# Optimization experiments

Measured on AMD Instinct MI355X. Metric: run time of the kernel, lower is better.

## Reference

```python
import jax, jax.numpy as jnp
import numpy as np

B, D, H = 32768, 512, 512


def setup_inputs() -> dict:
    key = jax.random.key(0)
    ks = jax.random.split(key, 20)
    stdv = 1.0 / np.sqrt(H)

    def u(k, shape):
        return jax.random.uniform(k, shape, jnp.float32, -stdv, stdv)

    inp = {
        "input": jax.random.normal(ks[0], (B, D), jnp.float32),
        "h": jax.random.normal(ks[1], (B, H), jnp.float32),
        "c": jax.random.normal(ks[2], (B, H), jnp.float32),
    }
    names = ["w_ii", "w_hi", "b_ii", "b_hi", "w_if", "w_hf", "b_if", "b_hf",
             "w_ig", "w_hg", "b_ig", "b_hg", "w_io", "w_ho", "b_io", "b_ho"]
    shapes = {"w_i": (D, H), "w_h": (H, H), "b_": (H,)}
    for i, n in enumerate(names):
        shp = (D, H) if n.startswith("w_i") else ((H, H) if n.startswith("w_h") else (H,))
        inp[n] = u(ks[3 + i], shp)
    return inp


def lstm_cell(input, h, c,
              w_ii, w_hi, b_ii, b_hi, w_if, w_hf, b_if, b_hf,
              w_ig, w_hg, b_ig, b_hg, w_io, w_ho, b_io, b_ho):
    # Fuse the 8 small GEMMs into 2 concatenated GEMMs: [B,D]@[D,4H], [B,H]@[H,4H].
    w_x = jnp.concatenate([w_ii, w_if, w_ig, w_io], axis=1)   # [D, 4H]
    w_h = jnp.concatenate([w_hi, w_hf, w_hg, w_ho], axis=1)   # [H, 4H]
    b = jnp.concatenate([b_ii + b_hi, b_if + b_hf, b_ig + b_hg, b_io + b_ho])  # [4H]
    pre = input @ w_x + h @ w_h + b                            # [B, 4H]
    i, f, g, o = jnp.split(pre, 4, axis=1)
    i = jax.nn.sigmoid(i)
    f = jax.nn.sigmoid(f)
    g = jax.nn.sigmoid(g)  # NOTE: source code uses sigmoid here (docstring says tanh)
    o = jax.nn.sigmoid(o)
    c_prime = f * c + i * g
    h_prime = o * jnp.tanh(c_prime)
    return h_prime, c_prime


def reference(input, h, c,
              w_ii, w_hi, b_ii, b_hi, w_if, w_hf, b_if, b_hf,
              w_ig, w_hg, b_ig, b_hg, w_io, w_ho, b_io, b_ho):
    return lstm_cell(input, h, c,
                     w_ii, w_hi, b_ii, b_hi, w_if, w_hf, b_if, b_hf,
                     w_ig, w_hg, b_ig, b_hg, w_io, w_ho, b_io, b_ho)
```

## Files before the change

### kernel.cpp

```cpp
#include <hip/hip_runtime.h>
#include <hip/hip_bf16.h>

typedef __attribute__((ext_vector_type(8))) __bf16 bf16x8;
typedef __attribute__((ext_vector_type(4))) float f32x4;

#define NB 32768
#define HDIM 512
#define KDIM 1024

struct WPtrs { const float* wi[4]; const float* wh[4]; };
struct BPtrs { const float* bi[4]; const float* bh[4]; };

__device__ __forceinline__ float fsigmoid(float x) {
  return 1.0f / (1.0f + __expf(-x));
}
__device__ __forceinline__ float ftanh(float x) {
  return 2.0f / (1.0f + __expf(-2.0f * x)) - 1.0f;
}
__device__ __forceinline__ bf16x8 pack8(float4 a, float4 b) {
  bf16x8 r;
  r[0] = (__bf16)a.x; r[1] = (__bf16)a.y; r[2] = (__bf16)a.z; r[3] = (__bf16)a.w;
  r[4] = (__bf16)b.x; r[5] = (__bf16)b.y; r[6] = (__bf16)b.z; r[7] = (__bf16)b.w;
  return r;
}
__device__ __forceinline__ void gll16(const void* g, void* l) {
  __builtin_amdgcn_global_load_lds(
      (const __attribute__((address_space(1))) void*)g,
      (__attribute__((address_space(3))) void*)l, 16, 0, 0);
}
#define MFMA16(A, B, C) \
  C = __builtin_amdgcn_mfma_f32_16x16x32_bf16(A, B, C, 0, 0, 0)

__global__ void pack_bias_kernel(BPtrs p, float* __restrict__ bias) {
  int idx = blockIdx.x * 256 + threadIdx.x;
  int g = idx >> 9, np = idx & 511;
  bias[idx] = p.bi[g][np] + p.bh[g][np];
}

__global__ void conv_a_kernel(const float* __restrict__ x,
                              const float* __restrict__ h,
                              __bf16* __restrict__ Abf) {
  const size_t N8 = (size_t)NB * KDIM / 8;
  for (size_t i = (size_t)blockIdx.x * blockDim.x + threadIdx.x; i < N8;
       i += (size_t)gridDim.x * blockDim.x) {
    size_t e = i * 8;
    int k = (int)(e & (KDIM - 1));
    size_t r = e >> 10;
    const float* s = (k < 512) ? (x + r * 512 + k) : (h + r * 512 + (k - 512));
    float4 v0 = *(const float4*)s;
    float4 v1 = *(const float4*)(s + 4);
    *(bf16x8*)(Abf + e) = pack8(v0, v1);
  }
}

__global__ void pack_w2_kernel(WPtrs p, __bf16* __restrict__ Wt) {
  __shared__ float tile[64][65];
  const int kt = blockIdx.x;
  const int nt = blockIdx.y;
  const int g = blockIdx.z;
  const int k0 = kt * 64, n0 = nt * 64;
  const float* src = (k0 < 512) ? p.wi[g] : p.wh[g];
  const int k0l = (k0 < 512) ? k0 : (k0 - 512);
  const int rr = threadIdx.x >> 6;
  const int cc = threadIdx.x & 63;
#pragma unroll
  for (int pp = 0; pp < 16; ++pp) {
    int kk = pp * 4 + rr;
    tile[kk][cc] = src[(size_t)(k0l + kk) * 512 + (n0 + cc)];
  }
  __syncthreads();
#pragma unroll
  for (int pp = 0; pp < 16; ++pp) {
    int nn = pp * 4 + rr;
    int np = n0 + nn;
    int prow = (np >> 6) * 256 + ((g >> 1) << 7) + (((np >> 4) & 3) << 5) +
               ((g & 1) << 4) + (np & 15);
    Wt[(size_t)prow * KDIM + (k0 + cc)] = (__bf16)tile[cc][nn];
  }
}

__global__ __launch_bounds__(512, 1) void lstm_gemm3(
    const __bf16* __restrict__ Abf, const __bf16* __restrict__ Wt,
    const float* __restrict__ cin, const float* __restrict__ bias,
    float* __restrict__ out) {
  __shared__ alignas(16) char lds[131072];
  const int tid = threadIdx.x;
  const int wid = tid >> 6;
  const int wm = wid >> 2, wn = wid & 3;
  const int lane = tid & 63;
  const int fc = lane & 15, fg = lane >> 4;

  const int bn = blockIdx.x & 7;
  const int bmg = blockIdx.x >> 3;

  const __bf16* Bsrc = Wt + (size_t)bn * 256 * KDIM;

  const int r0 = tid >> 3;
  const int ssl = ((tid & 7) ^ (r0 & 7)) * 8;
  const uint32_t ldst0 = (uint32_t)(tid >> 6) * 1024;

  f32x4 acc[8][4];
#pragma unroll
  for (int m = 0; m < 8; ++m)
#pragma unroll
    for (int n = 0; n < 4; ++n) acc[m][n] = (f32x4){0.f, 0.f, 0.f, 0.f};

  bf16x8 a[4][2], b0[2][2], b1[2][2];

  auto stA = [&](int t, int h) {
    if (t < 64) {
      const __bf16* g = Abf +
                        ((size_t)((bmg << 2) + (t >> 4)) * 256 + h * 128 + r0) *
                            KDIM +
                        (t & 15) * 64 + ssl;
      uint32_t lb = (uint32_t)(t & 1) * 65536 + (uint32_t)h * 16384 + ldst0;
      gll16(g, (void*)&lds[lb]);
      gll16(g + (size_t)64 * KDIM, (void*)&lds[lb + 8192]);
    }
  };
  auto stB = [&](int t, int h) {
    if (t < 64) {
      const __bf16* g =
          Bsrc + ((size_t)h * 128 + r0) * KDIM + (t & 15) * 64 + ssl;
      uint32_t lb =
          (uint32_t)(t & 1) * 65536 + 32768 + (uint32_t)h * 16384 + ldst0;
      gll16(g, (void*)&lds[lb]);
      gll16(g + (size_t)64 * KDIM, (void*)&lds[lb + 8192]);
    }
  };
  auto ldA = [&](int cb, int h, int mq, int ks) -> bf16x8 {
    int row = wm * 64 + mq * 16 + fc;
    uint32_t off = (uint32_t)cb * 65536 + (uint32_t)h * 16384 +
                   (uint32_t)row * 128 +
                   (uint32_t)(((ks * 4 + fg) ^ (row & 7)) << 4);
    return *(const bf16x8*)&lds[off];
  };
  auto ldB = [&](int cb, int h, int nq, int ks) -> bf16x8 {
    int row = wn * 32 + nq * 16 + fc;
    uint32_t off = (uint32_t)cb * 65536 + 32768 + (uint32_t)h * 16384 +
                   (uint32_t)row * 128 +
                   (uint32_t)(((ks * 4 + fg) ^ (row & 7)) << 4);
    return *(const bf16x8*)&lds[off];
  };

  const int np = bn * 64 + wn * 16 + fc;
  const float bi = bias[np];
  const float bf_ = bias[512 + np];
  const float bg = bias[1024 + np];
  const float bo = bias[1536 + np];
  const size_t couts = (size_t)NB * HDIM;

  stA(0, 0); stB(0, 0); stB(0, 1); stA(0, 1);
  stA(1, 0); stB(1, 0); stB(1, 1);
  asm volatile("s_waitcnt vmcnt(6)" ::: "memory");
  __builtin_amdgcn_s_barrier();

#pragma unroll 2
  for (int t = 0; t < 64; ++t) {
    const int cb = t & 1;
#pragma unroll
    for (int mq = 0; mq < 4; ++mq)
#pragma unroll
      for (int ks = 0; ks < 2; ++ks) a[mq][ks] = ldA(cb, 0, mq, ks);
#pragma unroll
    for (int nq = 0; nq < 2; ++nq)
#pragma unroll
      for (int ks = 0; ks < 2; ++ks) b0[nq][ks] = ldB(cb, 0, nq, ks);
    stA(t + 1, 1);
    __builtin_amdgcn_s_barrier();
    asm volatile("s_waitcnt lgkmcnt(0)" ::: "memory");
    __builtin_amdgcn_s_setprio(1);
#pragma unroll
    for (int mq = 0; mq < 4; ++mq)
#pragma unroll
      for (int nq = 0; nq < 2; ++nq)
#pragma unroll
        for (int ks = 0; ks < 2; ++ks)
          MFMA16(a[mq][ks], b0[nq][ks], acc[mq][nq]);
    __builtin_amdgcn_s_setprio(0);
    __builtin_amdgcn_s_barrier();
#pragma unroll
    for (int nq = 0; nq < 2; ++nq)
#pragma unroll
      for (int ks = 0; ks < 2; ++ks) b1[nq][ks] = ldB(cb, 1, nq, ks);
    stA(t + 2, 0);
    __builtin_amdgcn_s_barrier();
    asm volatile("s_waitcnt lgkmcnt(0)" ::: "memory");
    __builtin_amdgcn_s_setprio(1);
#pragma unroll
    for (int mq = 0; mq < 4; ++mq)
#pragma unroll
      for (int nq = 0; nq < 2; ++nq)
#pragma unroll
        for (int ks = 0; ks < 2; ++ks)
          MFMA16(a[mq][ks], b1[nq][ks], acc[mq][2 + nq]);
    __builtin_amdgcn_s_setprio(0);
    __builtin_amdgcn_s_barrier();
#pragma unroll
    for (int mq = 0; mq < 4; ++mq)
#pragma unroll
      for (int ks = 0; ks < 2; ++ks) a[mq][ks] = ldA(cb, 1, mq, ks);
    stB(t + 2, 0);
    __builtin_amdgcn_s_barrier();
    asm volatile("s_waitcnt lgkmcnt(0)" ::: "memory");
    __builtin_amdgcn_s_setprio(1);
#pragma unroll
    for (int mq = 0; mq < 4; ++mq)
#pragma unroll
      for (int nq = 0; nq < 2; ++nq)
#pragma unroll
        for (int ks = 0; ks < 2; ++ks)
          MFMA16(a[mq][ks], b1[nq][ks], acc[4 + mq][2 + nq]);
    __builtin_amdgcn_s_setprio(0);
    __builtin_amdgcn_s_barrier();
    stB(t + 2, 1);
    if (t < 62) {
      asm volatile("s_waitcnt vmcnt(6)" ::: "memory");
    } else if (t == 62) {
      asm volatile("s_waitcnt vmcnt(0)" ::: "memory");
    }
    __builtin_amdgcn_s_barrier();
    __builtin_amdgcn_s_setprio(1);
#pragma unroll
    for (int mq = 0; mq < 4; ++mq)
#pragma unroll
      for (int nq = 0; nq < 2; ++nq)
#pragma unroll
        for (int ks = 0; ks < 2; ++ks)
          MFMA16(a[mq][ks], b0[nq][ks], acc[4 + mq][nq]);
    __builtin_amdgcn_s_setprio(0);
    __builtin_amdgcn_s_barrier();

    if ((t & 15) == 15) {
      const int g = t >> 4;
#pragma unroll
      for (int mf = 0; mf < 8; ++mf) {
        const int grow0 = ((bmg << 2) + g) * 256 + (mf >> 2) * 128 + wm * 64 +
                          (mf & 3) * 16 + fg * 4;
#pragma unroll
        for (int j = 0; j < 4; ++j) {
          const size_t off = (size_t)(grow0 + j) * HDIM + np;
          float i_ = fsigmoid(acc[mf][0][j] + bi);
          float f_ = fsigmoid(acc[mf][1][j] + bf_);
          float g_ = fsigmoid(acc[mf][2][j] + bg);
          float o_ = fsigmoid(acc[mf][3][j] + bo);
          float cp = f_ * cin[off] + i_ * g_;
          out[off] = o_ * ftanh(cp);
          out[couts + off] = cp;
        }
#pragma unroll
        for (int n = 0; n < 4; ++n) acc[mf][n] = (f32x4){0.f, 0.f, 0.f, 0.f};
      }
    }
  }
}

extern "C" void kernel_launch(void* const* d_in, const int* in_sizes, int n_in,
                              void* d_out, int out_size, void* d_ws,
                              size_t ws_size, hipStream_t stream) {
  const float* xin = (const float*)d_in[0];
  const float* hin = (const float*)d_in[1];
  const float* cin = (const float*)d_in[2];
  WPtrs wp;
  wp.wi[0] = (const float*)d_in[3];
  wp.wi[1] = (const float*)d_in[7];
  wp.wi[2] = (const float*)d_in[11];
  wp.wi[3] = (const float*)d_in[15];
  wp.wh[0] = (const float*)d_in[4];
  wp.wh[1] = (const float*)d_in[8];
  wp.wh[2] = (const float*)d_in[12];
  wp.wh[3] = (const float*)d_in[16];
  BPtrs bp;
  bp.bi[0] = (const float*)d_in[5];
  bp.bi[1] = (const float*)d_in[9];
  bp.bi[2] = (const float*)d_in[13];
  bp.bi[3] = (const float*)d_in[17];
  bp.bh[0] = (const float*)d_in[6];
  bp.bh[1] = (const float*)d_in[10];
  bp.bh[2] = (const float*)d_in[14];
  bp.bh[3] = (const float*)d_in[18];

  const size_t needA = (size_t)NB * KDIM * 2;
  const size_t needW = (size_t)2048 * KDIM * 2;

  __bf16* Abf = (__bf16*)d_ws;
  __bf16* Wt = (__bf16*)((char*)d_ws + needA);
  float* bias = (float*)((char*)d_ws + needA + needW);

  conv_a_kernel<<<2048, 256, 0, stream>>>(xin, hin, Abf);
  pack_w2_kernel<<<dim3(16, 8, 4), 256, 0, stream>>>(wp, Wt);
  pack_bias_kernel<<<8, 256, 0, stream>>>(bp, bias);
  lstm_gemm3<<<256, 512, 0, stream>>>(Abf, Wt, cin, bias, (float*)d_out);
}
```

Baseline: 213.8 us.

## Restructure GEMM main loop with partial lgkmcnt waits and fewer barriers

Reorders the LDS fragment loads in the main GEMM loop so both B halves are loaded up front, then splits each MFMA phase into halves gated by partial lgkmcnt waits so compute starts before all LDS reads land. Several workgroup barriers are removed or replaced with scheduler barriers to cut synchronisation stalls per iteration. This raises register pressure (b0 and b1 live together) and relies on correct hazard ordering between LDS writes from global_load_lds and reads, which could risk races if a barrier was load-bearing.

```diff
diff --git a/kernel.cpp b/kernel.cpp
--- a/kernel.cpp
+++ b/kernel.cpp
@@ -30,6 +30,8 @@
 }
 #define MFMA16(A, B, C) \
   C = __builtin_amdgcn_mfma_f32_16x16x32_bf16(A, B, C, 0, 0, 0)
+#define SBAR() __builtin_amdgcn_s_barrier()
+#define SCHED0() __builtin_amdgcn_sched_barrier(0)
 
 __global__ void pack_bias_kernel(BPtrs p, float* __restrict__ bias) {
   int idx = blockIdx.x * 256 + threadIdx.x;
@@ -79,7 +81,7 @@
   }
 }
 
-__global__ __launch_bounds__(512, 1) void lstm_gemm3(
+__global__ __launch_bounds__(512, 1) void lstm_gemm4(
     const __bf16* __restrict__ Abf, const __bf16* __restrict__ Wt,
     const float* __restrict__ cin, const float* __restrict__ bias,
     float* __restrict__ out) {
@@ -153,22 +155,50 @@
   stA(0, 0); stB(0, 0); stB(0, 1); stA(0, 1);
   stA(1, 0); stB(1, 0); stB(1, 1);
   asm volatile("s_waitcnt vmcnt(6)" ::: "memory");
-  __builtin_amdgcn_s_barrier();
+  SBAR();
 
 #pragma unroll 2
   for (int t = 0; t < 64; ++t) {
     const int cb = t & 1;
 #pragma unroll
+    for (int nq = 0; nq < 2; ++nq)
+#pragma unroll
+      for (int ks = 0; ks < 2; ++ks) b0[nq][ks] = ldB(cb, 0, nq, ks);
+#pragma unroll
     for (int mq = 0; mq < 4; ++mq)
 #pragma unroll
       for (int ks = 0; ks < 2; ++ks) a[mq][ks] = ldA(cb, 0, mq, ks);
 #pragma unroll
     for (int nq = 0; nq < 2; ++nq)
 #pragma unroll
-      for (int ks = 0; ks < 2; ++ks) b0[nq][ks] = ldB(cb, 0, nq, ks);
+      for (int ks = 0; ks < 2; ++ks) b1[nq][ks] = ldB(cb, 1, nq, ks);
     stA(t + 1, 1);
-    __builtin_amdgcn_s_barrier();
+    asm volatile("s_waitcnt lgkmcnt(8)" ::: "memory");
+    SCHED0();
+    __builtin_amdgcn_s_setprio(1);
+#pragma unroll
+    for (int mq = 0; mq < 2; ++mq)
+#pragma unroll
+      for (int nq = 0; nq < 2; ++nq)
+#pragma unroll
+        for (int ks = 0; ks < 2; ++ks)
+          MFMA16(a[mq][ks], b0[nq][ks], acc[mq][nq]);
+    __builtin_amdgcn_s_setprio(0);
+    asm volatile("s_waitcnt lgkmcnt(4)" ::: "memory");
+    SCHED0();
+    __builtin_amdgcn_s_setprio(1);
+#pragma unroll
+    for (int mq = 2; mq < 4; ++mq)
+#pragma unroll
+      for (int nq = 0; nq < 2; ++nq)
+#pragma unroll
+        for (int ks = 0; ks < 2; ++ks)
+          MFMA16(a[mq][ks], b0[nq][ks], acc[mq][nq]);
+    __builtin_amdgcn_s_setprio(0);
+    SBAR();
+    stA(t + 2, 0);
     asm volatile("s_waitcnt lgkmcnt(0)" ::: "memory");
+    SCHED0();
     __builtin_amdgcn_s_setprio(1);
 #pragma unroll
     for (int mq = 0; mq < 4; ++mq)
@@ -176,50 +206,45 @@
       for (int nq = 0; nq < 2; ++nq)
 #pragma unroll
         for (int ks = 0; ks < 2; ++ks)
-          MFMA16(a[mq][ks], b0[nq][ks], acc[mq][nq]);
-    __builtin_amdgcn_s_setprio(0);
-    __builtin_amdgcn_s_barrier();
-#pragma unroll
-    for (int nq = 0; nq < 2; ++nq)
-#pragma unroll
-      for (int ks = 0; ks < 2; ++ks) b1[nq][ks] = ldB(cb, 1, nq, ks);
-    stA(t + 2, 0);
-    __builtin_amdgcn_s_barrier();
+          MFMA16(a[mq][ks], b1[nq][ks], acc[mq][2 + nq]);
+    __builtin_amdgcn_s_setprio(0);
+#pragma unroll
+    for (int mq = 0; mq < 4; ++mq)
+#pragma unroll
+      for (int ks = 0; ks < 2; ++ks) a[mq][ks] = ldA(cb, 1, mq, ks);
+    SCHED0();
+    SBAR();
+    stB(t + 2, 0);
+    asm volatile("s_waitcnt lgkmcnt(4)" ::: "memory");
+    SCHED0();
+    __builtin_amdgcn_s_setprio(1);
+#pragma unroll
+    for (int mq = 0; mq < 2; ++mq)
+#pragma unroll
+      for (int nq = 0; nq < 2; ++nq)
+#pragma unroll
+        for (int ks = 0; ks < 2; ++ks)
+          MFMA16(a[mq][ks], b1[nq][ks], acc[4 + mq][2 + nq]);
+    __builtin_amdgcn_s_setprio(0);
     asm volatile("s_waitcnt lgkmcnt(0)" ::: "memory");
-    __builtin_amdgcn_s_setprio(1);
-#pragma unroll
-    for (int mq = 0; mq < 4; ++mq)
-#pragma unroll
-      for (int nq = 0; nq < 2; ++nq)
-#pragma unroll
-        for (int ks = 0; ks < 2; ++ks)
-          MFMA16(a[mq][ks], b1[nq][ks], acc[mq][2 + nq]);
-    __builtin_amdgcn_s_setprio(0);
-    __builtin_amdgcn_s_barrier();
-#pragma unroll
-    for (int mq = 0; mq < 4; ++mq)
-#pragma unroll
-      for (int ks = 0; ks < 2; ++ks) a[mq][ks] = ldA(cb, 1, mq, ks);
-    stB(t + 2, 0);
-    __builtin_amdgcn_s_barrier();
-    asm volatile("s_waitcnt lgkmcnt(0)" ::: "memory");
-    __builtin_amdgcn_s_setprio(1);
-#pragma unroll
-    for (int mq = 0; mq < 4; ++mq)
+    SCHED0();
+    __builtin_amdgcn_s_setprio(1);
+#pragma unroll
+    for (int mq = 2; mq < 4; ++mq)
 #pragma unroll
       for (int nq = 0; nq < 2; ++nq)
 #pragma unroll
         for (int ks = 0; ks < 2; ++ks)
           MFMA16(a[mq][ks], b1[nq][ks], acc[4 + mq][2 + nq]);
     __builtin_amdgcn_s_setprio(0);
-    __builtin_amdgcn_s_barrier();
+    SBAR();
     stB(t + 2, 1);
     if (t < 62) {
       asm volatile("s_waitcnt vmcnt(6)" ::: "memory");
     } else if (t == 62) {
       asm volatile("s_waitcnt vmcnt(0)" ::: "memory");
     }
-    __builtin_amdgcn_s_barrier();
+    SCHED0();
     __builtin_amdgcn_s_setprio(1);
 #pragma unroll
     for (int mq = 0; mq < 4; ++mq)
@@ -229,7 +254,7 @@
         for (int ks = 0; ks < 2; ++ks)
           MFMA16(a[mq][ks], b0[nq][ks], acc[4 + mq][nq]);
     __builtin_amdgcn_s_setprio(0);
-    __builtin_amdgcn_s_barrier();
+    SBAR();
 
     if ((t & 15) == 15) {
       const int g = t >> 4;
@@ -290,5 +315,5 @@
   conv_a_kernel<<<2048, 256, 0, stream>>>(xin, hin, Abf);
   pack_w2_kernel<<<dim3(16, 8, 4), 256, 0, stream>>>(wp, Wt);
   pack_bias_kernel<<<8, 256, 0, stream>>>(bp, bias);
-  lstm_gemm3<<<256, 512, 0, stream>>>(Abf, Wt, cin, bias, (float*)d_out);
-}
+  lstm_gemm4<<<256, 512, 0, stream>>>(Abf, Wt, cin, bias, (float*)d_out);
+}
```

After: 210.7 us. About the same (-1.5%).

## Restructure GEMM main loop to 4-stage K=32 pipeline with interleaved LDS reads

Applied to the files above, without the earlier changes.

Replaces the two-buffer K=64 pipeline, which had four barrier-separated MFMA phases per step, with a four-buffer ring of K=32 tiles. Each step has a single barrier, and A-fragment LDS reads are interleaved with MFMA groups using fine-grained lgkmcnt waits and sched_barrier. The aim is to cut barrier count and let LDS latency hide behind MFMAs, with global prefetches issued mid-loop two stages ahead. The LDS layout drops the XOR swizzle for a plain 64-byte row stride, which may bring bank conflicts.

```diff
diff --git a/kernel.cpp b/kernel.cpp
--- a/kernel.cpp
+++ b/kernel.cpp
@@ -30,6 +30,8 @@
 }
 #define MFMA16(A, B, C) \
   C = __builtin_amdgcn_mfma_f32_16x16x32_bf16(A, B, C, 0, 0, 0)
+#define SBAR() __builtin_amdgcn_s_barrier()
+#define SCHED0() __builtin_amdgcn_sched_barrier(0)
 
 __global__ void pack_bias_kernel(BPtrs p, float* __restrict__ bias) {
   int idx = blockIdx.x * 256 + threadIdx.x;
@@ -79,7 +81,7 @@
   }
 }
 
-__global__ __launch_bounds__(512, 1) void lstm_gemm3(
+__global__ __launch_bounds__(512, 1) void lstm_gemm6(
     const __bf16* __restrict__ Abf, const __bf16* __restrict__ Wt,
     const float* __restrict__ cin, const float* __restrict__ bias,
     float* __restrict__ out) {
@@ -93,11 +95,10 @@
   const int bn = blockIdx.x & 7;
   const int bmg = blockIdx.x >> 3;
 
-  const __bf16* Bsrc = Wt + (size_t)bn * 256 * KDIM;
-
-  const int r0 = tid >> 3;
-  const int ssl = ((tid & 7) ^ (r0 & 7)) * 8;
-  const uint32_t ldst0 = (uint32_t)(tid >> 6) * 1024;
+  const __bf16* Bsrc = Wt + (size_t)(bn * 256) * KDIM;
+
+  const int srow = (wid << 4) + (lane >> 2);
+  const int skoff = (lane & 3) * 8;
 
   f32x4 acc[8][4];
 #pragma unroll
@@ -105,42 +106,36 @@
 #pragma unroll
     for (int n = 0; n < 4; ++n) acc[m][n] = (f32x4){0.f, 0.f, 0.f, 0.f};
 
-  bf16x8 a[4][2], b0[2][2], b1[2][2];
-
-  auto stA = [&](int t, int h) {
-    if (t < 64) {
-      const __bf16* g = Abf +
-                        ((size_t)((bmg << 2) + (t >> 4)) * 256 + h * 128 + r0) *
-                            KDIM +
-                        (t & 15) * 64 + ssl;
-      uint32_t lb = (uint32_t)(t & 1) * 65536 + (uint32_t)h * 16384 + ldst0;
-      gll16(g, (void*)&lds[lb]);
-      gll16(g + (size_t)64 * KDIM, (void*)&lds[lb + 8192]);
-    }
-  };
-  auto stB = [&](int t, int h) {
-    if (t < 64) {
-      const __bf16* g =
-          Bsrc + ((size_t)h * 128 + r0) * KDIM + (t & 15) * 64 + ssl;
-      uint32_t lb =
-          (uint32_t)(t & 1) * 65536 + 32768 + (uint32_t)h * 16384 + ldst0;
-      gll16(g, (void*)&lds[lb]);
-      gll16(g + (size_t)64 * KDIM, (void*)&lds[lb + 8192]);
-    }
-  };
-  auto ldA = [&](int cb, int h, int mq, int ks) -> bf16x8 {
-    int row = wm * 64 + mq * 16 + fc;
-    uint32_t off = (uint32_t)cb * 65536 + (uint32_t)h * 16384 +
-                   (uint32_t)row * 128 +
-                   (uint32_t)(((ks * 4 + fg) ^ (row & 7)) << 4);
-    return *(const bf16x8*)&lds[off];
-  };
-  auto ldB = [&](int cb, int h, int nq, int ks) -> bf16x8 {
-    int row = wn * 32 + nq * 16 + fc;
-    uint32_t off = (uint32_t)cb * 65536 + 32768 + (uint32_t)h * 16384 +
-                   (uint32_t)row * 128 +
-                   (uint32_t)(((ks * 4 + fg) ^ (row & 7)) << 4);
-    return *(const bf16x8*)&lds[off];
+  bf16x8 a[2], b[4];
+
+  auto stA = [&](int t) {
+    if (t < 128) {
+      const __bf16* s = Abf +
+                        ((size_t)((bmg << 2) + (t >> 5)) * 256 + srow) * KDIM +
+                        (t & 31) * 32 + skoff;
+      uint32_t lb = (uint32_t)(t & 3) * 32768 + (uint32_t)wid * 1024;
+      gll16(s, (void*)&lds[lb]);
+      gll16(s + (size_t)128 * KDIM, (void*)&lds[lb + 8192]);
+    }
+  };
+  auto stB = [&](int t) {
+    if (t < 128) {
+      const __bf16* s = Bsrc + (size_t)srow * KDIM + (t & 31) * 32 + skoff;
+      uint32_t lb = (uint32_t)(t & 3) * 32768 + 16384 + (uint32_t)wid * 1024;
+      gll16(s, (void*)&lds[lb]);
+      gll16(s + (size_t)128 * KDIM, (void*)&lds[lb + 8192]);
+    }
+  };
+  auto ldA = [&](uint32_t t3, int mq) -> bf16x8 {
+    return *(const bf16x8*)&lds[t3 +
+                                (uint32_t)(wm * 128 + mq * 16 + fc) * 64 +
+                                (uint32_t)fg * 16];
+  };
+  auto ldB = [&](uint32_t t3, int nq) -> bf16x8 {
+    return *(const bf16x8*)&lds[t3 + 16384 +
+                                (uint32_t)((nq >> 1) * 128 + wn * 32 +
+                                           (nq & 1) * 16 + fc) * 64 +
+                                (uint32_t)fg * 16];
   };
 
   const int np = bn * 64 + wn * 16 + fc;
@@ -150,93 +145,49 @@
   const float bo = bias[1536 + np];
   const size_t couts = (size_t)NB * HDIM;
 
-  stA(0, 0); stB(0, 0); stB(0, 1); stA(0, 1);
-  stA(1, 0); stB(1, 0); stB(1, 1);
-  asm volatile("s_waitcnt vmcnt(6)" ::: "memory");
-  __builtin_amdgcn_s_barrier();
-
-#pragma unroll 2
-  for (int t = 0; t < 64; ++t) {
-    const int cb = t & 1;
-#pragma unroll
-    for (int mq = 0; mq < 4; ++mq)
-#pragma unroll
-      for (int ks = 0; ks < 2; ++ks) a[mq][ks] = ldA(cb, 0, mq, ks);
-#pragma unroll
-    for (int nq = 0; nq < 2; ++nq)
-#pragma unroll
-      for (int ks = 0; ks < 2; ++ks) b0[nq][ks] = ldB(cb, 0, nq, ks);
-    stA(t + 1, 1);
-    __builtin_amdgcn_s_barrier();
-    asm volatile("s_waitcnt lgkmcnt(0)" ::: "memory");
-    __builtin_amdgcn_s_setprio(1);
-#pragma unroll
-    for (int mq = 0; mq < 4; ++mq)
-#pragma unroll
-      for (int nq = 0; nq < 2; ++nq)
-#pragma unroll
-        for (int ks = 0; ks < 2; ++ks)
-          MFMA16(a[mq][ks], b0[nq][ks], acc[mq][nq]);
-    __builtin_amdgcn_s_setprio(0);
-    __builtin_amdgcn_s_barrier();
-#pragma unroll
-    for (int nq = 0; nq < 2; ++nq)
-#pragma unroll
-      for (int ks = 0; ks < 2; ++ks) b1[nq][ks] = ldB(cb, 1, nq, ks);
-    stA(t + 2, 0);
-    __builtin_amdgcn_s_barrier();
-    asm volatile("s_waitcnt lgkmcnt(0)" ::: "memory");
-    __builtin_amdgcn_s_setprio(1);
-#pragma unroll
-    for (int mq = 0; mq < 4; ++mq)
-#pragma unroll
-      for (int nq = 0; nq < 2; ++nq)
-#pragma unroll
-        for (int ks = 0; ks < 2; ++ks)
-          MFMA16(a[mq][ks], b1[nq][ks], acc[mq][2 + nq]);
-    __builtin_amdgcn_s_setprio(0);
-    __builtin_amdgcn_s_barrier();
-#pragma unroll
-    for (int mq = 0; mq < 4; ++mq)
-#pragma unroll
-      for (int ks = 0; ks < 2; ++ks) a[mq][ks] = ldA(cb, 1, mq, ks);
-    stB(t + 2, 0);
-    __builtin_amdgcn_s_barrier();
-    asm volatile("s_waitcnt lgkmcnt(0)" ::: "memory");
-    __builtin_amdgcn_s_setprio(1);
-#pragma unroll
-    for (int mq = 0; mq < 4; ++mq)
-#pragma unroll
-      for (int nq = 0; nq < 2; ++nq)
-#pragma unroll
-        for (int ks = 0; ks < 2; ++ks)
-          MFMA16(a[mq][ks], b1[nq][ks], acc[4 + mq][2 + nq]);
-    __builtin_amdgcn_s_setprio(0);
-    __builtin_amdgcn_s_barrier();
-    stB(t + 2, 1);
-    if (t < 62) {
-      asm volatile("s_waitcnt vmcnt(6)" ::: "memory");
-    } else if (t == 62) {
+  stA(0); stB(0); stA(1); stB(1);
+  asm volatile("s_waitcnt vmcnt(4)" ::: "memory");
+  SBAR();
+
+#pragma unroll 4
+  for (int t = 0; t < 128; ++t) {
+    const uint32_t t3 = (uint32_t)(t & 3) * 32768;
+    a[0] = ldA(t3, 0);
+    b[0] = ldB(t3, 0);
+    b[1] = ldB(t3, 1);
+    b[2] = ldB(t3, 2);
+    b[3] = ldB(t3, 3);
+    a[1] = ldA(t3, 1);
+#pragma unroll
+    for (int mq = 0; mq < 8; ++mq) {
+      if (mq < 7) {
+        asm volatile("s_waitcnt lgkmcnt(1)" ::: "memory");
+      } else {
+        asm volatile("s_waitcnt lgkmcnt(0)" ::: "memory");
+      }
+      SCHED0();
+      __builtin_amdgcn_s_setprio(1);
+      MFMA16(a[mq & 1], b[0], acc[mq][0]);
+      MFMA16(a[mq & 1], b[1], acc[mq][1]);
+      MFMA16(a[mq & 1], b[2], acc[mq][2]);
+      MFMA16(a[mq & 1], b[3], acc[mq][3]);
+      __builtin_amdgcn_s_setprio(0);
+      if (mq < 6) a[mq & 1] = ldA(t3, mq + 2);
+      if (mq == 2) stA(t + 2);
+      if (mq == 4) stB(t + 2);
+    }
+    if (t < 126) {
+      asm volatile("s_waitcnt vmcnt(4)" ::: "memory");
+    } else if (t == 126) {
       asm volatile("s_waitcnt vmcnt(0)" ::: "memory");
     }
-    __builtin_amdgcn_s_barrier();
-    __builtin_amdgcn_s_setprio(1);
-#pragma unroll
-    for (int mq = 0; mq < 4; ++mq)
-#pragma unroll
-      for (int nq = 0; nq < 2; ++nq)
-#pragma unroll
-        for (int ks = 0; ks < 2; ++ks)
-          MFMA16(a[mq][ks], b0[nq][ks], acc[4 + mq][nq]);
-    __builtin_amdgcn_s_setprio(0);
-    __builtin_amdgcn_s_barrier();
-
-    if ((t & 15) == 15) {
-      const int g = t >> 4;
+    SBAR();
+
+    if ((t & 31) == 31) {
+      const int grp = t >> 5;
 #pragma unroll
       for (int mf = 0; mf < 8; ++mf) {
-        const int grow0 = ((bmg << 2) + g) * 256 + (mf >> 2) * 128 + wm * 64 +
-                          (mf & 3) * 16 + fg * 4;
+        const int grow0 = ((bmg << 2) + grp) * 256 + wm * 128 + mf * 16 + fg * 4;
 #pragma unroll
         for (int j = 0; j < 4; ++j) {
           const size_t off = (size_t)(grow0 + j) * HDIM + np;
@@ -290,5 +241,5 @@
   conv_a_kernel<<<2048, 256, 0, stream>>>(xin, hin, Abf);
   pack_w2_kernel<<<dim3(16, 8, 4), 256, 0, stream>>>(wp, Wt);
   pack_bias_kernel<<<8, 256, 0, stream>>>(bp, bias);
-  lstm_gemm3<<<256, 512, 0, stream>>>(Abf, Wt, cin, bias, (float*)d_out);
-}
+  lstm_gemm6<<<256, 512, 0, stream>>>(Abf, Wt, cin, bias, (float*)d_out);
+}
```

Measured after the change: 213.8 us. Within noise of the previous version (+0.0%).

## Switch GEMM to 32x32x16 MFMA with 4x2 wave tiling and simpler pipeline

Applied to the files above, without the earlier changes.

Replaces the 16x16x32 bf16 MFMA tiles with 32x32x16 MFMAs and changes the wave layout from 2x4 to 4x2. Each wave now covers 64 rows and 32 columns across all four gates. The weight packing permutation is adjusted so each 32-column group holds all four gates contiguously. The main loop is restructured to issue global-to-LDS loads for the next tile in one stage, interleave LDS reads with MFMAs using lgkmcnt waits, and use a single barrier per iteration instead of many. The aim is fewer LDS reads per FLOP and less barrier overhead. The cost is reduced prefetch depth (one tile ahead, with a full vmcnt(0) wait every iteration) and a different epilogue row mapping.

```diff
diff --git a/kernel.cpp b/kernel.cpp
--- a/kernel.cpp
+++ b/kernel.cpp
@@ -3,6 +3,7 @@
 
 typedef __attribute__((ext_vector_type(8))) __bf16 bf16x8;
 typedef __attribute__((ext_vector_type(4))) float f32x4;
+typedef __attribute__((ext_vector_type(16))) float f32x16;
 
 #define NB 32768
 #define HDIM 512
@@ -28,8 +29,12 @@
       (const __attribute__((address_space(1))) void*)g,
       (__attribute__((address_space(3))) void*)l, 16, 0, 0);
 }
-#define MFMA16(A, B, C) \
-  C = __builtin_amdgcn_mfma_f32_16x16x32_bf16(A, B, C, 0, 0, 0)
+#define MFMA32(A, B, C) \
+  C = __builtin_amdgcn_mfma_f32_32x32x16_bf16(A, B, C, 0, 0, 0)
+#define SBAR() __builtin_amdgcn_s_barrier()
+#define SCHED0() __builtin_amdgcn_sched_barrier(0)
+#define LGKM(n) asm volatile("s_waitcnt lgkmcnt(" #n ")" ::: "memory")
+#define VMCNT0() asm volatile("s_waitcnt vmcnt(0)" ::: "memory")
 
 __global__ void pack_bias_kernel(BPtrs p, float* __restrict__ bias) {
   int idx = blockIdx.x * 256 + threadIdx.x;
@@ -53,7 +58,7 @@
   }
 }
 
-__global__ void pack_w2_kernel(WPtrs p, __bf16* __restrict__ Wt) {
+__global__ void pack_w1_kernel(WPtrs p, __bf16* __restrict__ Wt) {
   __shared__ float tile[64][65];
   const int kt = blockIdx.x;
   const int nt = blockIdx.y;
@@ -73,39 +78,40 @@
   for (int pp = 0; pp < 16; ++pp) {
     int nn = pp * 4 + rr;
     int np = n0 + nn;
-    int prow = (np >> 6) * 256 + ((g >> 1) << 7) + (((np >> 4) & 3) << 5) +
-               ((g & 1) << 4) + (np & 15);
+    int prow = ((np >> 5) << 7) + g * 32 + (np & 31);
     Wt[(size_t)prow * KDIM + (k0 + cc)] = (__bf16)tile[cc][nn];
   }
 }
 
-__global__ __launch_bounds__(512, 1) void lstm_gemm3(
+__global__ __launch_bounds__(512, 1) void lstm_gemm9(
     const __bf16* __restrict__ Abf, const __bf16* __restrict__ Wt,
     const float* __restrict__ cin, const float* __restrict__ bias,
     float* __restrict__ out) {
   __shared__ alignas(16) char lds[131072];
   const int tid = threadIdx.x;
   const int wid = tid >> 6;
-  const int wm = wid >> 2, wn = wid & 3;
+  const int wm = wid >> 1, wn = wid & 1;
   const int lane = tid & 63;
-  const int fc = lane & 15, fg = lane >> 4;
+  const int l31 = lane & 31, kg = lane >> 5;
 
   const int bn = blockIdx.x & 7;
   const int bmg = blockIdx.x >> 3;
 
-  const __bf16* Bsrc = Wt + (size_t)bn * 256 * KDIM;
+  const __bf16* Bsrc = Wt + (size_t)(bn * 256) * KDIM;
 
   const int r0 = tid >> 3;
   const int ssl = ((tid & 7) ^ (r0 & 7)) * 8;
-  const uint32_t ldst0 = (uint32_t)(tid >> 6) * 1024;
-
-  f32x4 acc[8][4];
-#pragma unroll
-  for (int m = 0; m < 8; ++m)
-#pragma unroll
-    for (int n = 0; n < 4; ++n) acc[m][n] = (f32x4){0.f, 0.f, 0.f, 0.f};
-
-  bf16x8 a[4][2], b0[2][2], b1[2][2];
+  const uint32_t ldst0 = (uint32_t)wid * 1024;
+
+  f32x16 acc[2][4];
+#pragma unroll
+  for (int m = 0; m < 2; ++m)
+#pragma unroll
+    for (int g = 0; g < 4; ++g)
+#pragma unroll
+      for (int r = 0; r < 16; ++r) acc[m][g][r] = 0.f;
+
+  bf16x8 aa[2][2], bb[2][4];
 
   auto stA = [&](int t, int h) {
     if (t < 64) {
@@ -128,128 +134,103 @@
       gll16(g + (size_t)64 * KDIM, (void*)&lds[lb + 8192]);
     }
   };
-  auto ldA = [&](int cb, int h, int mq, int ks) -> bf16x8 {
-    int row = wm * 64 + mq * 16 + fc;
+  auto ldA = [&](int cb, int m, int ks) -> bf16x8 {
+    int row = wm * 64 + m * 32 + l31;
+    int h = row >> 7, lr = row & 127;
     uint32_t off = (uint32_t)cb * 65536 + (uint32_t)h * 16384 +
-                   (uint32_t)row * 128 +
-                   (uint32_t)(((ks * 4 + fg) ^ (row & 7)) << 4);
+                   (uint32_t)lr * 128 +
+                   (uint32_t)(((ks * 2 + kg) ^ (lr & 7)) << 4);
     return *(const bf16x8*)&lds[off];
   };
-  auto ldB = [&](int cb, int h, int nq, int ks) -> bf16x8 {
-    int row = wn * 32 + nq * 16 + fc;
-    uint32_t off = (uint32_t)cb * 65536 + 32768 + (uint32_t)h * 16384 +
-                   (uint32_t)row * 128 +
-                   (uint32_t)(((ks * 4 + fg) ^ (row & 7)) << 4);
+  auto ldB = [&](int cb, int g, int ks) -> bf16x8 {
+    int lr = g * 32 + l31;
+    uint32_t off = (uint32_t)cb * 65536 + 32768 + (uint32_t)wn * 16384 +
+                   (uint32_t)lr * 128 +
+                   (uint32_t)(((ks * 2 + kg) ^ (lr & 7)) << 4);
     return *(const bf16x8*)&lds[off];
   };
 
-  const int np = bn * 64 + wn * 16 + fc;
+  const int np = bn * 64 + wn * 32 + l31;
   const float bi = bias[np];
   const float bf_ = bias[512 + np];
   const float bg = bias[1024 + np];
   const float bo = bias[1536 + np];
   const size_t couts = (size_t)NB * HDIM;
 
-  stA(0, 0); stB(0, 0); stB(0, 1); stA(0, 1);
-  stA(1, 0); stB(1, 0); stB(1, 1);
-  asm volatile("s_waitcnt vmcnt(6)" ::: "memory");
-  __builtin_amdgcn_s_barrier();
+  stA(0, 0); stA(0, 1); stB(0, 0); stB(0, 1);
+  VMCNT0();
+  SBAR();
 
 #pragma unroll 2
   for (int t = 0; t < 64; ++t) {
     const int cb = t & 1;
-#pragma unroll
-    for (int mq = 0; mq < 4; ++mq)
-#pragma unroll
-      for (int ks = 0; ks < 2; ++ks) a[mq][ks] = ldA(cb, 0, mq, ks);
-#pragma unroll
-    for (int nq = 0; nq < 2; ++nq)
-#pragma unroll
-      for (int ks = 0; ks < 2; ++ks) b0[nq][ks] = ldB(cb, 0, nq, ks);
-    stA(t + 1, 1);
-    __builtin_amdgcn_s_barrier();
-    asm volatile("s_waitcnt lgkmcnt(0)" ::: "memory");
-    __builtin_amdgcn_s_setprio(1);
-#pragma unroll
-    for (int mq = 0; mq < 4; ++mq)
-#pragma unroll
-      for (int nq = 0; nq < 2; ++nq)
-#pragma unroll
-        for (int ks = 0; ks < 2; ++ks)
-          MFMA16(a[mq][ks], b0[nq][ks], acc[mq][nq]);
-    __builtin_amdgcn_s_setprio(0);
-    __builtin_amdgcn_s_barrier();
-#pragma unroll
-    for (int nq = 0; nq < 2; ++nq)
-#pragma unroll
-      for (int ks = 0; ks < 2; ++ks) b1[nq][ks] = ldB(cb, 1, nq, ks);
-    stA(t + 2, 0);
-    __builtin_amdgcn_s_barrier();
-    asm volatile("s_waitcnt lgkmcnt(0)" ::: "memory");
-    __builtin_amdgcn_s_setprio(1);
-#pragma unroll
-    for (int mq = 0; mq < 4; ++mq)
-#pragma unroll
-      for (int nq = 0; nq < 2; ++nq)
-#pragma unroll
-        for (int ks = 0; ks < 2; ++ks)
-          MFMA16(a[mq][ks], b1[nq][ks], acc[mq][2 + nq]);
-    __builtin_amdgcn_s_setprio(0);
-    __builtin_amdgcn_s_barrier();
-#pragma unroll
-    for (int mq = 0; mq < 4; ++mq)
-#pragma unroll
-      for (int ks = 0; ks < 2; ++ks) a[mq][ks] = ldA(cb, 1, mq, ks);
-    stB(t + 2, 0);
-    __builtin_amdgcn_s_barrier();
-    asm volatile("s_waitcnt lgkmcnt(0)" ::: "memory");
-    __builtin_amdgcn_s_setprio(1);
-#pragma unroll
-    for (int mq = 0; mq < 4; ++mq)
-#pragma unroll
-      for (int nq = 0; nq < 2; ++nq)
-#pragma unroll
-        for (int ks = 0; ks < 2; ++ks)
-          MFMA16(a[mq][ks], b1[nq][ks], acc[4 + mq][2 + nq]);
-    __builtin_amdgcn_s_setprio(0);
-    __builtin_amdgcn_s_barrier();
-    stB(t + 2, 1);
-    if (t < 62) {
-      asm volatile("s_waitcnt vmcnt(6)" ::: "memory");
-    } else if (t == 62) {
-      asm volatile("s_waitcnt vmcnt(0)" ::: "memory");
-    }
-    __builtin_amdgcn_s_barrier();
-    __builtin_amdgcn_s_setprio(1);
-#pragma unroll
-    for (int mq = 0; mq < 4; ++mq)
-#pragma unroll
-      for (int nq = 0; nq < 2; ++nq)
-#pragma unroll
-        for (int ks = 0; ks < 2; ++ks)
-          MFMA16(a[mq][ks], b0[nq][ks], acc[4 + mq][nq]);
-    __builtin_amdgcn_s_setprio(0);
-    __builtin_amdgcn_s_barrier();
+    bb[0][0] = ldB(cb, 0, 0); bb[0][1] = ldB(cb, 1, 0);
+    bb[0][2] = ldB(cb, 2, 0); bb[0][3] = ldB(cb, 3, 0);
+    aa[0][0] = ldA(cb, 0, 0); aa[0][1] = ldA(cb, 1, 0);
+    bb[1][0] = ldB(cb, 0, 1); bb[1][1] = ldB(cb, 1, 1);
+    bb[1][2] = ldB(cb, 2, 1); bb[1][3] = ldB(cb, 3, 1);
+    aa[1][0] = ldA(cb, 0, 1); aa[1][1] = ldA(cb, 1, 1);
+    stA(t + 1, 0); stA(t + 1, 1);
+    LGKM(6); SCHED0();
+    __builtin_amdgcn_s_setprio(1);
+#pragma unroll
+    for (int m = 0; m < 2; ++m)
+#pragma unroll
+      for (int g = 0; g < 4; ++g) MFMA32(aa[0][m], bb[0][g], acc[m][g]);
+    __builtin_amdgcn_s_setprio(0);
+    bb[0][0] = ldB(cb, 0, 2); bb[0][1] = ldB(cb, 1, 2);
+    bb[0][2] = ldB(cb, 2, 2); bb[0][3] = ldB(cb, 3, 2);
+    aa[0][0] = ldA(cb, 0, 2); aa[0][1] = ldA(cb, 1, 2);
+    stB(t + 1, 0);
+    LGKM(6); SCHED0();
+    __builtin_amdgcn_s_setprio(1);
+#pragma unroll
+    for (int m = 0; m < 2; ++m)
+#pragma unroll
+      for (int g = 0; g < 4; ++g) MFMA32(aa[1][m], bb[1][g], acc[m][g]);
+    __builtin_amdgcn_s_setprio(0);
+    bb[1][0] = ldB(cb, 0, 3); bb[1][1] = ldB(cb, 1, 3);
+    bb[1][2] = ldB(cb, 2, 3); bb[1][3] = ldB(cb, 3, 3);
+    aa[1][0] = ldA(cb, 0, 3); aa[1][1] = ldA(cb, 1, 3);
+    stB(t + 1, 1);
+    LGKM(6); SCHED0();
+    __builtin_amdgcn_s_setprio(1);
+#pragma unroll
+    for (int m = 0; m < 2; ++m)
+#pragma unroll
+      for (int g = 0; g < 4; ++g) MFMA32(aa[0][m], bb[0][g], acc[m][g]);
+    __builtin_amdgcn_s_setprio(0);
+    LGKM(0); VMCNT0(); SCHED0();
+    __builtin_amdgcn_s_setprio(1);
+#pragma unroll
+    for (int m = 0; m < 2; ++m)
+#pragma unroll
+      for (int g = 0; g < 4; ++g) MFMA32(aa[1][m], bb[1][g], acc[m][g]);
+    __builtin_amdgcn_s_setprio(0);
+    SBAR();
 
     if ((t & 15) == 15) {
-      const int g = t >> 4;
-#pragma unroll
-      for (int mf = 0; mf < 8; ++mf) {
-        const int grow0 = ((bmg << 2) + g) * 256 + (mf >> 2) * 128 + wm * 64 +
-                          (mf & 3) * 16 + fg * 4;
-#pragma unroll
-        for (int j = 0; j < 4; ++j) {
-          const size_t off = (size_t)(grow0 + j) * HDIM + np;
-          float i_ = fsigmoid(acc[mf][0][j] + bi);
-          float f_ = fsigmoid(acc[mf][1][j] + bf_);
-          float g_ = fsigmoid(acc[mf][2][j] + bg);
-          float o_ = fsigmoid(acc[mf][3][j] + bo);
+      const int grp = t >> 4;
+#pragma unroll
+      for (int m = 0; m < 2; ++m) {
+        const int rowbase =
+            ((bmg << 2) + grp) * 256 + wm * 64 + m * 32 + kg * 4;
+#pragma unroll
+        for (int r = 0; r < 16; ++r) {
+          const int row = rowbase + (r & 3) + 8 * (r >> 2);
+          const size_t off = (size_t)row * HDIM + np;
+          float i_ = fsigmoid(acc[m][0][r] + bi);
+          float f_ = fsigmoid(acc[m][1][r] + bf_);
+          float g_ = fsigmoid(acc[m][2][r] + bg);
+          float o_ = fsigmoid(acc[m][3][r] + bo);
           float cp = f_ * cin[off] + i_ * g_;
           out[off] = o_ * ftanh(cp);
           out[couts + off] = cp;
         }
 #pragma unroll
-        for (int n = 0; n < 4; ++n) acc[mf][n] = (f32x4){0.f, 0.f, 0.f, 0.f};
+        for (int g = 0; g < 4; ++g)
+#pragma unroll
+          for (int r = 0; r < 16; ++r) acc[m][g][r] = 0.f;
       }
     }
   }
@@ -288,7 +269,7 @@
   float* bias = (float*)((char*)d_ws + needA + needW);
 
   conv_a_kernel<<<2048, 256, 0, stream>>>(xin, hin, Abf);
-  pack_w2_kernel<<<dim3(16, 8, 4), 256, 0, stream>>>(wp, Wt);
+  pack_w1_kernel<<<dim3(16, 8, 4), 256, 0, stream>>>(wp, Wt);
   pack_bias_kernel<<<8, 256, 0, stream>>>(bp, bias);
-  lstm_gemm3<<<256, 512, 0, stream>>>(Abf, Wt, cin, bias, (float*)d_out);
-}
+  lstm_gemm9<<<256, 512, 0, stream>>>(Abf, Wt, cin, bias, (float*)d_out);
+}
```

After: 222.6 us. +4.1%, slower.
